# Optimization experiments

Hardware: AMD Instinct MI355X
Metric: run time of the kernel (lower is better)

Reference implementation:

```python
import jax, jax.numpy as jnp
import numpy as np

D_MODEL = 1024
NUM_HEADS = 16


def setup_inputs() -> dict:
    key = jax.random.key(0)
    ks = jax.random.split(key, 5)
    B, S, D = 2, 2048, D_MODEL
    x = jax.random.normal(ks[0], (B, S, D), dtype=jnp.float32)
    # nn.Linear(d_model, d_model, bias=False) weights, shape [out, in]
    scale = 1.0 / np.sqrt(D)
    Wq = jax.random.normal(ks[1], (D, D), dtype=jnp.float32) * scale
    Wk = jax.random.normal(ks[2], (D, D), dtype=jnp.float32) * scale
    Wv = jax.random.normal(ks[3], (D, D), dtype=jnp.float32) * scale
    Wo = jax.random.normal(ks[4], (D, D), dtype=jnp.float32) * scale
    return {"x": x, "Wq": Wq, "Wk": Wk, "Wv": Wv, "Wo": Wo}


def reference(x, Wq, Wk, Wv, Wo):
    B, S, D = x.shape
    H = NUM_HEADS
    dh = D // H
    # projections: x @ W.T (Linear without bias)
    q = (x @ Wq.T).reshape(B, S, H, dh).transpose(0, 2, 1, 3)  # [B,H,S,dh]
    k = (x @ Wk.T).reshape(B, S, H, dh).transpose(0, 2, 1, 3)
    v = (x @ Wv.T).reshape(B, S, H, dh).transpose(0, 2, 1, 3)
    scores = jnp.einsum("bhqd,bhkd->bhqk", q, k) / jnp.sqrt(jnp.float32(dh))
    # causal mask: positions j > i get -inf before softmax
    causal = jnp.triu(jnp.ones((S, S), dtype=bool), k=1)
    scores = jnp.where(causal, -jnp.inf, scores)
    attn = jax.nn.softmax(scores, axis=-1)  # [B,H,S,S]
    out = jnp.einsum("bhqk,bhkd->bhqd", attn, v)  # [B,H,S,dh]
    out = out.transpose(0, 2, 1, 3).reshape(B, S, D)
    return out @ Wo.T
```

## Files before the change

### kernel.cpp

```cpp
#include <hip/hip_runtime.h>

typedef __attribute__((ext_vector_type(8))) __bf16 bf16x8;
typedef __attribute__((ext_vector_type(4))) __bf16 bf16x4;
typedef __attribute__((ext_vector_type(2))) __bf16 bf16x2;
typedef __attribute__((ext_vector_type(4))) float f32x4;
typedef __attribute__((ext_vector_type(16))) float f32x16;
typedef __attribute__((ext_vector_type(4))) unsigned uint4v;

static constexpr int S = 2048;
static constexpr int D = 1024;
static constexpr int BATCH = 2;
static constexpr int M_ROWS = BATCH * S;

#define GLOAD_LDS16(gp, lp)                                                        \
  __builtin_amdgcn_global_load_lds((const __attribute__((address_space(1))) void*)(gp), \
                                   (__attribute__((address_space(3))) void*)(lp), 16, 0, 0)

__global__ __launch_bounds__(256) void cast_f32_bf16(const float* __restrict__ in,
                                                     __bf16* __restrict__ out) {
  int i = (blockIdx.x * 256 + threadIdx.x) * 4;
  *reinterpret_cast<bf16x4*>(out + i) =
      __builtin_convertvector(*reinterpret_cast<const f32x4*>(in + i), bf16x4);
}

__global__ __launch_bounds__(256) void cast_w4(const float* __restrict__ w0, const float* __restrict__ w1,
                                               const float* __restrict__ w2, const float* __restrict__ w3,
                                               __bf16* __restrict__ o0, __bf16* __restrict__ o1,
                                               __bf16* __restrict__ o2, __bf16* __restrict__ o3) {
  const float* in = blockIdx.y == 0 ? w0 : blockIdx.y == 1 ? w1 : blockIdx.y == 2 ? w2 : w3;
  __bf16* out = blockIdx.y == 0 ? o0 : blockIdx.y == 1 ? o1 : blockIdx.y == 2 ? o2 : o3;
  int i = (blockIdx.x * 256 + threadIdx.x) * 4;
  *reinterpret_cast<bf16x4*>(out + i) =
      __builtin_convertvector(*reinterpret_cast<const f32x4*>(in + i), bf16x4);
}

template <typename OutT>
__device__ __forceinline__ void gemm_core(const __bf16* __restrict__ A,
                                          const __bf16* __restrict__ Bm,
                                          OutT* __restrict__ C, int m0, int n0, int K, int ldc,
                                          __bf16* At, __bf16* Bt) {
  const int tid = threadIdx.x;
  const int w = tid >> 6, l = tid & 63;
  const int wr = w >> 1, wc = w & 1;
  const int ln = l & 15, gr = l >> 4;

  const int srow = w * 32 + (l >> 2);
  const int scol = (l & 3) * 8;
  const size_t aoff = (size_t)(m0 + srow) * K + scol;
  const size_t boff = (size_t)(n0 + srow) * K + scol;
  __bf16* lA = At + w * 2 * 512;
  __bf16* lB = Bt + w * 2 * 512;

  f32x4 acc[4][4] = {};

  for (int k0 = 0; k0 < K; k0 += 32) {
    __syncthreads();
    GLOAD_LDS16(A + aoff + k0, lA);
    GLOAD_LDS16(A + aoff + (size_t)16 * K + k0, lA + 512);
    GLOAD_LDS16(Bm + boff + k0, lB);
    GLOAD_LDS16(Bm + boff + (size_t)16 * K + k0, lB + 512);
    __syncthreads();

    bf16x8 af[4], bfr[4];
#pragma unroll
    for (int mi = 0; mi < 4; mi++)
      af[mi] = *reinterpret_cast<const bf16x8*>(&At[(wr * 64 + mi * 16 + ln) * 32 + gr * 8]);
#pragma unroll
    for (int ni = 0; ni < 4; ni++)
      bfr[ni] = *reinterpret_cast<const bf16x8*>(&Bt[(wc * 64 + ni * 16 + ln) * 32 + gr * 8]);
#pragma unroll
    for (int mi = 0; mi < 4; mi++)
#pragma unroll
      for (int ni = 0; ni < 4; ni++)
        acc[mi][ni] = __builtin_amdgcn_mfma_f32_16x16x32_bf16(af[mi], bfr[ni], acc[mi][ni], 0, 0, 0);
  }

#pragma unroll
  for (int mi = 0; mi < 4; mi++)
#pragma unroll
    for (int ni = 0; ni < 4; ni++)
#pragma unroll
      for (int r = 0; r < 4; r++) {
        int row = m0 + wr * 64 + mi * 16 + gr * 4 + r;
        int col = n0 + wc * 64 + ni * 16 + ln;
        float v = acc[mi][ni][r];
        if constexpr (__is_same(OutT, float))
          C[(size_t)row * ldc + col] = v;
        else
          C[(size_t)row * ldc + col] = (__bf16)v;
      }
}

__global__ __launch_bounds__(256) void qkv_gemm(const __bf16* __restrict__ xb,
                                                const __bf16* __restrict__ wq,
                                                const __bf16* __restrict__ wk,
                                                const __bf16* __restrict__ wv,
                                                __bf16* __restrict__ q, __bf16* __restrict__ k,
                                                __bf16* __restrict__ vt) {
  __shared__ __bf16 At[128 * 32];
  __shared__ __bf16 Bt[128 * 32];
  const int id = blockIdx.x;
  const __bf16 *A, *B;
  __bf16* C;
  int m0, n0, ldc;
  if (id < 512) {
    A = xb;
    B = (id < 256) ? wq : wk;
    C = (id < 256) ? q : k;
    int t = id & 255;
    m0 = (t >> 3) * 128;
    n0 = (t & 7) * 128;
    ldc = 1024;
  } else {
    int t = id - 512;
    A = wv;
    B = xb;
    C = vt;
    m0 = (t & 7) * 128;
    n0 = (t >> 3) * 128;
    ldc = 4096;
  }
  gemm_core<__bf16>(A, B, C, m0, n0, 1024, ldc, At, Bt);
}

__global__ __launch_bounds__(256) void wo_gemm(const __bf16* __restrict__ ob,
                                               const __bf16* __restrict__ wo,
                                               float* __restrict__ out) {
  __shared__ __bf16 At[128 * 32];
  __shared__ __bf16 Bt[128 * 32];
  gemm_core<float>(ob, wo, out, blockIdx.y * 128, blockIdx.x * 128, 1024, 1024, At, Bt);
}

__global__ __launch_bounds__(512, 2) void attn_kernel(const __bf16* __restrict__ Qb,
                                                      const __bf16* __restrict__ Kb,
                                                      const __bf16* __restrict__ VTb,
                                                      __bf16* __restrict__ Ob) {
  const int lin = blockIdx.x;
  const int wid = ((lin & 7) << 5) | (lin >> 3);
  const int bh = wid >> 3;
  const int j = wid & 7;
  const int b = bh >> 4, h = bh & 15;

  const int tid = threadIdx.x;
  const int w = tid >> 6, l = tid & 63;
  const int q31 = l & 31, hi = l >> 5;

  int qt;
  switch (w) {
    case 0: qt = j; break;
    case 1: qt = 16 + j; break;
    case 2: qt = 15 - j; break;
    case 3: qt = 31 - j; break;
    case 4: qt = 63 - j; break;
    case 5: qt = 47 - j; break;
    case 6: qt = 48 + j; break;
    default: qt = 32 + j; break;
  }
  const int q0 = qt * 32;
  const int n = qt + 1;

  const __bf16* Qp = Qb + (size_t)b * S * D + h * 64;
  const __bf16* Kp = Kb + (size_t)b * S * D + h * 64;
  const __bf16* Vt = VTb + (size_t)(h * 64) * M_ROWS + b * S;

  const float SCALE2 = 0.125f * 1.44269504f;
  const float NEG = -1e30f;
  const float THR_RAW = 8.0f / SCALE2;

  bf16x8 qf[4];
#pragma unroll
  for (int ds = 0; ds < 4; ds++)
    qf[ds] = *reinterpret_cast<const bf16x8*>(
        Qp + (size_t)(q0 + q31) * D + ds * 16 + hi * 8);

  f32x16 oacc[2] = {};
  float mr = NEG, ls = 0.f;

  auto loadK = [&](bf16x8 (&dst)[4], int kk) {
#pragma unroll
    for (int ds = 0; ds < 4; ds++)
      dst[ds] = *reinterpret_cast<const bf16x8*>(
          Kp + (size_t)(kk + q31) * D + ds * 16 + hi * 8);
  };
  auto loadV = [&](bf16x8 (&dst)[2][2], int kk) {
#pragma unroll
    for (int d0 = 0; d0 < 2; d0++)
#pragma unroll
      for (int ks = 0; ks < 2; ks++)
        dst[d0][ks] = *reinterpret_cast<const bf16x8*>(
            Vt + (size_t)(d0 * 32 + q31) * M_ROWS + kk + ks * 16 + hi * 8);
  };
  auto qk = [&](f32x16& st, bf16x8 (&kf)[4]) {
    f32x16 z = {};
    __builtin_amdgcn_s_setprio(1);
#pragma unroll
    for (int ds = 0; ds < 4; ds++)
      z = __builtin_amdgcn_mfma_f32_32x32x16_bf16(kf[ds], qf[ds], z, 0, 0, 0);
    __builtin_amdgcn_s_setprio(0);
    st = z;
  };

  auto pack2 = [](float x, float y) -> unsigned {
    bf16x2 p;
    p[0] = (__bf16)x;
    p[1] = (__bf16)y;
    return __builtin_bit_cast(unsigned, p);
  };

  auto smpv = [&](f32x16& st, bf16x8 (&vf)[2][2], int t) {
    const bool tail = (t == n - 1);
    float pv[16];
#pragma unroll
    for (int r = 0; r < 16; r++) {
      float v = st[r];
      if (tail) {
        int keyidx = (r & 3) + 8 * (r >> 2) + 4 * hi;
        v = (keyidx <= q31) ? v : NEG;
      }
      pv[r] = v;
    }
    float t8[8], t4[4];
#pragma unroll
    for (int i = 0; i < 8; i++) t8[i] = fmaxf(pv[i], pv[i + 8]);
#pragma unroll
    for (int i = 0; i < 4; i++) t4[i] = fmaxf(t8[i], t8[i + 4]);
    float tm = fmaxf(fmaxf(t4[0], t4[1]), fmaxf(t4[2], t4[3]));
    tm = fmaxf(tm, __shfl_xor(tm, 32));
    if (!__all(tm - mr <= THR_RAW)) {
      float nm = fmaxf(mr, tm);
      float a = __builtin_exp2f((mr - nm) * SCALE2);
      mr = nm;
      ls *= a;
#pragma unroll
      for (int d0 = 0; d0 < 2; d0++)
#pragma unroll
        for (int r = 0; r < 16; r++) oacc[d0][r] *= a;
    }
    const float mrs = mr * SCALE2;
#pragma unroll
    for (int r = 0; r < 16; r++)
      pv[r] = __builtin_exp2f(__builtin_fmaf(pv[r], SCALE2, -mrs));
    float s8[8], s4[4];
#pragma unroll
    for (int i = 0; i < 8; i++) s8[i] = pv[i] + pv[i + 8];
#pragma unroll
    for (int i = 0; i < 4; i++) s4[i] = s8[i] + s8[i + 4];
    float ps = (s4[0] + s4[1]) + (s4[2] + s4[3]);
    ps += __shfl_xor(ps, 32);
    ls += ps;

    unsigned dw[8];
#pragma unroll
    for (int bb = 0; bb < 4; bb++) {
      dw[2 * bb] = pack2(pv[4 * bb], pv[4 * bb + 1]);
      dw[2 * bb + 1] = pack2(pv[4 * bb + 2], pv[4 * bb + 3]);
    }
    __builtin_amdgcn_s_setprio(1);
#pragma unroll
    for (int ks = 0; ks < 2; ks++) {
      unsigned s0 = hi ? dw[4 * ks + 0] : dw[4 * ks + 2];
      unsigned s1 = hi ? dw[4 * ks + 1] : dw[4 * ks + 3];
      unsigned r0 = (unsigned)__shfl_xor((int)s0, 32);
      unsigned r1 = (unsigned)__shfl_xor((int)s1, 32);
      uint4v uv;
      uv.x = hi ? r0 : dw[4 * ks + 0];
      uv.y = hi ? r1 : dw[4 * ks + 1];
      uv.z = hi ? dw[4 * ks + 2] : r0;
      uv.w = hi ? dw[4 * ks + 3] : r1;
      bf16x8 pb = __builtin_bit_cast(bf16x8, uv);
      oacc[0] = __builtin_amdgcn_mfma_f32_32x32x16_bf16(vf[0][ks], pb, oacc[0], 0, 0, 0);
      oacc[1] = __builtin_amdgcn_mfma_f32_32x32x16_bf16(vf[1][ks], pb, oacc[1], 0, 0, 0);
    }
    __builtin_amdgcn_s_setprio(0);
  };

  f32x16 stA, stB;
  bf16x8 kf0[4], kf1[4], vf0[2][2], vf1[2][2];

  loadK(kf0, 0);
  loadV(vf0, 0);
  if (n > 1) {
    loadK(kf1, 32);
    loadV(vf1, 32);
  }
  qk(stA, kf0);

  auto iter_step = [&](f32x16& stCur, f32x16& stNxt, bf16x8 (&kfNxt)[4],
                       bf16x8 (&kfTgt)[4], bf16x8 (&vfCur)[2][2], int t) {
    if (t + 1 < n) qk(stNxt, kfNxt);
    if (t + 2 < n) loadK(kfTgt, 32 * (t + 2));
    smpv(stCur, vfCur, t);
    if (t + 2 < n) loadV(vfCur, 32 * (t + 2));
  };

  int t = 0;
  for (;;) {
    iter_step(stA, stB, kf1, kf0, vf0, t);
    if (++t >= n) break;
    iter_step(stB, stA, kf0, kf1, vf1, t);
    if (++t >= n) break;
  }

  {
    float inv = 1.0f / ls;
    size_t row = (size_t)(b * S + q0 + q31);
#pragma unroll
    for (int d0 = 0; d0 < 2; d0++)
#pragma unroll
      for (int bb = 0; bb < 4; bb++) {
        bf16x4 ov = {(__bf16)(oacc[d0][4 * bb + 0] * inv), (__bf16)(oacc[d0][4 * bb + 1] * inv),
                     (__bf16)(oacc[d0][4 * bb + 2] * inv), (__bf16)(oacc[d0][4 * bb + 3] * inv)};
        *reinterpret_cast<bf16x4*>(Ob + row * D + h * 64 + d0 * 32 + 8 * bb + 4 * hi) = ov;
      }
  }
}

extern "C" void kernel_launch(void* const* d_in, const int* in_sizes, int n_in,
                              void* d_out, int out_size, void* d_ws, size_t ws_size,
                              hipStream_t stream) {
  const float* x = (const float*)d_in[0];
  const float* Wq = (const float*)d_in[1];
  const float* Wk = (const float*)d_in[2];
  const float* Wv = (const float*)d_in[3];
  const float* Wo = (const float*)d_in[4];
  float* out = (float*)d_out;

  char* ws = (char*)d_ws;
  const size_t MB = 1024 * 1024;
  __bf16* xb = (__bf16*)(ws + 0 * MB);
  __bf16* qb = (__bf16*)(ws + 8 * MB);
  __bf16* kb = (__bf16*)(ws + 16 * MB);
  __bf16* vtb = (__bf16*)(ws + 24 * MB);
  __bf16* ob = (__bf16*)(ws + 32 * MB);
  __bf16* wqb = (__bf16*)(ws + 40 * MB);
  __bf16* wkb = (__bf16*)(ws + 42 * MB);
  __bf16* wvb = (__bf16*)(ws + 44 * MB);
  __bf16* wob = (__bf16*)(ws + 46 * MB);

  const int nx = M_ROWS * D;
  const int nw = D * D;

  cast_f32_bf16<<<nx / 4 / 256, 256, 0, stream>>>(x, xb);
  cast_w4<<<dim3(nw / 4 / 256, 4), 256, 0, stream>>>(Wq, Wk, Wv, Wo, wqb, wkb, wvb, wob);

  qkv_gemm<<<768, 256, 0, stream>>>(xb, wqb, wkb, wvb, qb, kb, vtb);

  attn_kernel<<<256, 512, 0, stream>>>(qb, kb, vtb, ob);

  wo_gemm<<<dim3(8, 32), 256, 0, stream>>>(ob, wob, out);
}
```

Baseline: 147.7 us.

## Split each query tile's KV range across two waves and merge via LDS

Each attention query tile's key range is now split between two waves that each run online softmax over half of the key blocks. The halves' partial outputs, max and sum are combined through shared memory after a block barrier. The grid doubles to 512 blocks with 4 query tiles per block, and launch bounds are raised to 4 blocks per CU to add parallelism and shorten the per-wave critical path. In exchange it adds an LDS round trip, a __syncthreads, extra rescaling work, and tighter register pressure from the higher occupancy target.

```diff
diff --git a/kernel.cpp b/kernel.cpp
--- a/kernel.cpp
+++ b/kernel.cpp
@@ -131,33 +131,39 @@
   gemm_core<float>(ob, wo, out, blockIdx.y * 128, blockIdx.x * 128, 1024, 1024, At, Bt);
 }
 
-__global__ __launch_bounds__(512, 2) void attn_kernel(const __bf16* __restrict__ Qb,
+__global__ __launch_bounds__(512, 4) void attn_kernel(const __bf16* __restrict__ Qb,
                                                       const __bf16* __restrict__ Kb,
                                                       const __bf16* __restrict__ VTb,
                                                       __bf16* __restrict__ Ob) {
+  __shared__ float mlds[4][64][34];
+
   const int lin = blockIdx.x;
-  const int wid = ((lin & 7) << 5) | (lin >> 3);
-  const int bh = wid >> 3;
-  const int j = wid & 7;
+  const int xcd = lin & 7;
+  const int idx = lin >> 3;
+  const int bh = xcd * 4 + (idx >> 4);
+  const int i = idx & 15;
   const int b = bh >> 4, h = bh & 15;
 
   const int tid = threadIdx.x;
   const int w = tid >> 6, l = tid & 63;
   const int q31 = l & 31, hi = l >> 5;
 
-  int qt;
+  int qt, half, slot;
   switch (w) {
-    case 0: qt = j; break;
-    case 1: qt = 16 + j; break;
-    case 2: qt = 15 - j; break;
-    case 3: qt = 31 - j; break;
-    case 4: qt = 63 - j; break;
-    case 5: qt = 47 - j; break;
-    case 6: qt = 48 + j; break;
-    default: qt = 32 + j; break;
+    case 0: qt = 2 * i;      half = 0; slot = 0; break;
+    case 1: qt = 2 * i;      half = 1; slot = 0; break;
+    case 2: qt = 2 * i + 1;  half = 0; slot = 1; break;
+    case 3: qt = 2 * i + 1;  half = 1; slot = 1; break;
+    case 4: qt = 63 - 2 * i; half = 1; slot = 2; break;
+    case 5: qt = 63 - 2 * i; half = 0; slot = 2; break;
+    case 6: qt = 62 - 2 * i; half = 1; slot = 3; break;
+    default: qt = 62 - 2 * i; half = 0; slot = 3; break;
   }
   const int q0 = qt * 32;
   const int n = qt + 1;
+  const int n0 = (n + 1) >> 1;
+  const int s0 = half ? n0 : 0;
+  const int cnt = half ? (n - n0) : n0;
 
   const __bf16* Qp = Qb + (size_t)b * S * D + h * 64;
   const __bf16* Kp = Kb + (size_t)b * S * D + h * 64;
@@ -207,8 +213,7 @@
     return __builtin_bit_cast(unsigned, p);
   };
 
-  auto smpv = [&](f32x16& st, bf16x8 (&vf)[2][2], int t) {
-    const bool tail = (t == n - 1);
+  auto smpv = [&](f32x16& st, bf16x8 (&vf)[2][2], bool tail) {
     float pv[16];
 #pragma unroll
     for (int r = 0; r < 16; r++) {
@@ -221,9 +226,9 @@
     }
     float t8[8], t4[4];
 #pragma unroll
-    for (int i = 0; i < 8; i++) t8[i] = fmaxf(pv[i], pv[i + 8]);
-#pragma unroll
-    for (int i = 0; i < 4; i++) t4[i] = fmaxf(t8[i], t8[i + 4]);
+    for (int ii = 0; ii < 8; ii++) t8[ii] = fmaxf(pv[ii], pv[ii + 8]);
+#pragma unroll
+    for (int ii = 0; ii < 4; ii++) t4[ii] = fmaxf(t8[ii], t8[ii + 4]);
     float tm = fmaxf(fmaxf(t4[0], t4[1]), fmaxf(t4[2], t4[3]));
     tm = fmaxf(tm, __shfl_xor(tm, 32));
     if (!__all(tm - mr <= THR_RAW)) {
@@ -242,9 +247,9 @@
       pv[r] = __builtin_exp2f(__builtin_fmaf(pv[r], SCALE2, -mrs));
     float s8[8], s4[4];
 #pragma unroll
-    for (int i = 0; i < 8; i++) s8[i] = pv[i] + pv[i + 8];
-#pragma unroll
-    for (int i = 0; i < 4; i++) s4[i] = s8[i] + s8[i + 4];
+    for (int ii = 0; ii < 8; ii++) s8[ii] = pv[ii] + pv[ii + 8];
+#pragma unroll
+    for (int ii = 0; ii < 4; ii++) s4[ii] = s8[ii] + s8[ii + 4];
     float ps = (s4[0] + s4[1]) + (s4[2] + s4[3]);
     ps += __shfl_xor(ps, 32);
     ls += ps;
@@ -258,10 +263,10 @@
     __builtin_amdgcn_s_setprio(1);
 #pragma unroll
     for (int ks = 0; ks < 2; ks++) {
-      unsigned s0 = hi ? dw[4 * ks + 0] : dw[4 * ks + 2];
-      unsigned s1 = hi ? dw[4 * ks + 1] : dw[4 * ks + 3];
-      unsigned r0 = (unsigned)__shfl_xor((int)s0, 32);
-      unsigned r1 = (unsigned)__shfl_xor((int)s1, 32);
+      unsigned s0v = hi ? dw[4 * ks + 0] : dw[4 * ks + 2];
+      unsigned s1v = hi ? dw[4 * ks + 1] : dw[4 * ks + 3];
+      unsigned r0 = (unsigned)__shfl_xor((int)s0v, 32);
+      unsigned r1 = (unsigned)__shfl_xor((int)s1v, 32);
       uint4v uv;
       uv.x = hi ? r0 : dw[4 * ks + 0];
       uv.y = hi ? r1 : dw[4 * ks + 1];
@@ -277,39 +282,59 @@
   f32x16 stA, stB;
   bf16x8 kf0[4], kf1[4], vf0[2][2], vf1[2][2];
 
-  loadK(kf0, 0);
-  loadV(vf0, 0);
-  if (n > 1) {
-    loadK(kf1, 32);
-    loadV(vf1, 32);
-  }
-  qk(stA, kf0);
-
-  auto iter_step = [&](f32x16& stCur, f32x16& stNxt, bf16x8 (&kfNxt)[4],
-                       bf16x8 (&kfTgt)[4], bf16x8 (&vfCur)[2][2], int t) {
-    if (t + 1 < n) qk(stNxt, kfNxt);
-    if (t + 2 < n) loadK(kfTgt, 32 * (t + 2));
-    smpv(stCur, vfCur, t);
-    if (t + 2 < n) loadV(vfCur, 32 * (t + 2));
-  };
-
-  int t = 0;
-  for (;;) {
-    iter_step(stA, stB, kf1, kf0, vf0, t);
-    if (++t >= n) break;
-    iter_step(stB, stA, kf0, kf1, vf1, t);
-    if (++t >= n) break;
-  }
-
-  {
-    float inv = 1.0f / ls;
+  if (cnt > 0) {
+    loadK(kf0, s0 * 32);
+    loadV(vf0, s0 * 32);
+    if (cnt > 1) {
+      loadK(kf1, (s0 + 1) * 32);
+      loadV(vf1, (s0 + 1) * 32);
+    }
+    qk(stA, kf0);
+
+    auto iter_step = [&](f32x16& stCur, f32x16& stNxt, bf16x8 (&kfNxt)[4],
+                         bf16x8 (&kfTgt)[4], bf16x8 (&vfCur)[2][2], int t) {
+      if (t + 1 < cnt) qk(stNxt, kfNxt);
+      if (t + 2 < cnt) loadK(kfTgt, (s0 + t + 2) * 32);
+      smpv(stCur, vfCur, s0 + t == n - 1);
+      if (t + 2 < cnt) loadV(vfCur, (s0 + t + 2) * 32);
+    };
+
+    int t = 0;
+    for (;;) {
+      iter_step(stA, stB, kf1, kf0, vf0, t);
+      if (++t >= cnt) break;
+      iter_step(stB, stA, kf0, kf1, vf1, t);
+      if (++t >= cnt) break;
+    }
+  }
+
+  if (half == 1) {
+    float* p = &mlds[slot][l][0];
+#pragma unroll
+    for (int r = 0; r < 16; r++) p[r] = oacc[0][r];
+#pragma unroll
+    for (int r = 0; r < 16; r++) p[16 + r] = oacc[1][r];
+    p[32] = mr;
+    p[33] = ls;
+  }
+  __syncthreads();
+  if (half == 0) {
+    const float* p = &mlds[slot][l][0];
+    float mr1 = p[32], ls1 = p[33];
+    float mc = fmaxf(mr, mr1);
+    float a0 = __builtin_exp2f((mr - mc) * SCALE2);
+    float a1 = __builtin_exp2f((mr1 - mc) * SCALE2);
+    float inv = 1.0f / (ls * a0 + ls1 * a1);
+    float f0 = a0 * inv, f1 = a1 * inv;
     size_t row = (size_t)(b * S + q0 + q31);
 #pragma unroll
     for (int d0 = 0; d0 < 2; d0++)
 #pragma unroll
       for (int bb = 0; bb < 4; bb++) {
-        bf16x4 ov = {(__bf16)(oacc[d0][4 * bb + 0] * inv), (__bf16)(oacc[d0][4 * bb + 1] * inv),
-                     (__bf16)(oacc[d0][4 * bb + 2] * inv), (__bf16)(oacc[d0][4 * bb + 3] * inv)};
+        bf16x4 ov;
+#pragma unroll
+        for (int rr = 0; rr < 4; rr++)
+          ov[rr] = (__bf16)(oacc[d0][4 * bb + rr] * f0 + p[d0 * 16 + 4 * bb + rr] * f1);
         *reinterpret_cast<bf16x4*>(Ob + row * D + h * 64 + d0 * 32 + 8 * bb + 4 * hi) = ov;
       }
   }
@@ -345,7 +370,7 @@
 
   qkv_gemm<<<768, 256, 0, stream>>>(xb, wqb, wkb, wvb, qb, kb, vtb);
 
-  attn_kernel<<<256, 512, 0, stream>>>(qb, kb, vtb, ob);
+  attn_kernel<<<512, 512, 0, stream>>>(qb, kb, vtb, ob);
 
   wo_gemm<<<dim3(8, 32), 256, 0, stream>>>(ob, wob, out);
 }
```

Measured after the change: 347.5 us. 2.35x slower.

## Split causal key range into two independent online-softmax streams per wave

Applied to the files above, without the earlier changes.

Each wave now processes the key tiles as two halves with separate running max, sum and output accumulators. Each loop iteration handles one tile from each half, and the two partial results are merged with a log-sum-exp combine at the end. The goal is more instruction-level parallelism, since the two independent MFMA and softmax chains can interleave, replacing the earlier software-pipelined single stream. The cost is more registers for the doubled accumulators and fragments, which could lower occupancy or cause spills. Loads are also now issued just before use rather than a full iteration ahead.

```diff
diff --git a/kernel.cpp b/kernel.cpp
--- a/kernel.cpp
+++ b/kernel.cpp
@@ -158,6 +158,8 @@
   }
   const int q0 = qt * 32;
   const int n = qt + 1;
+  const int na = (n + 1) >> 1;
+  const int nb = n >> 1;
 
   const __bf16* Qp = Qb + (size_t)b * S * D + h * 64;
   const __bf16* Kp = Kb + (size_t)b * S * D + h * 64;
@@ -173,8 +175,8 @@
     qf[ds] = *reinterpret_cast<const bf16x8*>(
         Qp + (size_t)(q0 + q31) * D + ds * 16 + hi * 8);
 
-  f32x16 oacc[2] = {};
-  float mr = NEG, ls = 0.f;
+  f32x16 oaccA[2] = {}, oaccB[2] = {};
+  float mrA = NEG, lsA = 0.f, mrB = NEG, lsB = 0.f;
 
   auto loadK = [&](bf16x8 (&dst)[4], int kk) {
 #pragma unroll
@@ -190,26 +192,20 @@
         dst[d0][ks] = *reinterpret_cast<const bf16x8*>(
             Vt + (size_t)(d0 * 32 + q31) * M_ROWS + kk + ks * 16 + hi * 8);
   };
-  auto qk = [&](f32x16& st, bf16x8 (&kf)[4]) {
+  auto qk1 = [&](f32x16& st, bf16x8 (&kf)[4]) {
     f32x16 z = {};
-    __builtin_amdgcn_s_setprio(1);
 #pragma unroll
     for (int ds = 0; ds < 4; ds++)
       z = __builtin_amdgcn_mfma_f32_32x32x16_bf16(kf[ds], qf[ds], z, 0, 0, 0);
-    __builtin_amdgcn_s_setprio(0);
     st = z;
   };
-
   auto pack2 = [](float x, float y) -> unsigned {
     bf16x2 p;
     p[0] = (__bf16)x;
     p[1] = (__bf16)y;
     return __builtin_bit_cast(unsigned, p);
   };
-
-  auto smpv = [&](f32x16& st, bf16x8 (&vf)[2][2], int t) {
-    const bool tail = (t == n - 1);
-    float pv[16];
+  auto maskmax = [&](f32x16& st, bool tail, float (&pv)[16]) -> float {
 #pragma unroll
     for (int r = 0; r < 16; r++) {
       float v = st[r];
@@ -221,95 +217,121 @@
     }
     float t8[8], t4[4];
 #pragma unroll
-    for (int i = 0; i < 8; i++) t8[i] = fmaxf(pv[i], pv[i + 8]);
-#pragma unroll
-    for (int i = 0; i < 4; i++) t4[i] = fmaxf(t8[i], t8[i + 4]);
+    for (int ii = 0; ii < 8; ii++) t8[ii] = fmaxf(pv[ii], pv[ii + 8]);
+#pragma unroll
+    for (int ii = 0; ii < 4; ii++) t4[ii] = fmaxf(t8[ii], t8[ii + 4]);
     float tm = fmaxf(fmaxf(t4[0], t4[1]), fmaxf(t4[2], t4[3]));
-    tm = fmaxf(tm, __shfl_xor(tm, 32));
-    if (!__all(tm - mr <= THR_RAW)) {
-      float nm = fmaxf(mr, tm);
-      float a = __builtin_exp2f((mr - nm) * SCALE2);
-      mr = nm;
-      ls *= a;
-#pragma unroll
-      for (int d0 = 0; d0 < 2; d0++)
-#pragma unroll
-        for (int r = 0; r < 16; r++) oacc[d0][r] *= a;
-    }
+    return fmaxf(tm, __shfl_xor(tm, 32));
+  };
+  auto rescale = [&](float& mr, float& ls, f32x16& o0, f32x16& o1, float tm) {
+    float nm = fmaxf(mr, tm);
+    float a = __builtin_exp2f((mr - nm) * SCALE2);
+    mr = nm;
+    ls *= a;
+#pragma unroll
+    for (int r = 0; r < 16; r++) o0[r] *= a;
+#pragma unroll
+    for (int r = 0; r < 16; r++) o1[r] *= a;
+  };
+  auto expsum = [&](float (&pv)[16], float mr, float& ls, unsigned (&dw)[8]) {
     const float mrs = mr * SCALE2;
 #pragma unroll
     for (int r = 0; r < 16; r++)
       pv[r] = __builtin_exp2f(__builtin_fmaf(pv[r], SCALE2, -mrs));
     float s8[8], s4[4];
 #pragma unroll
-    for (int i = 0; i < 8; i++) s8[i] = pv[i] + pv[i + 8];
-#pragma unroll
-    for (int i = 0; i < 4; i++) s4[i] = s8[i] + s8[i + 4];
+    for (int ii = 0; ii < 8; ii++) s8[ii] = pv[ii] + pv[ii + 8];
+#pragma unroll
+    for (int ii = 0; ii < 4; ii++) s4[ii] = s8[ii] + s8[ii + 4];
     float ps = (s4[0] + s4[1]) + (s4[2] + s4[3]);
     ps += __shfl_xor(ps, 32);
     ls += ps;
-
-    unsigned dw[8];
 #pragma unroll
     for (int bb = 0; bb < 4; bb++) {
       dw[2 * bb] = pack2(pv[4 * bb], pv[4 * bb + 1]);
       dw[2 * bb + 1] = pack2(pv[4 * bb + 2], pv[4 * bb + 3]);
     }
-    __builtin_amdgcn_s_setprio(1);
+  };
+  auto pvmma = [&](unsigned (&dw)[8], bf16x8 (&vf)[2][2], f32x16& o0, f32x16& o1) {
 #pragma unroll
     for (int ks = 0; ks < 2; ks++) {
-      unsigned s0 = hi ? dw[4 * ks + 0] : dw[4 * ks + 2];
-      unsigned s1 = hi ? dw[4 * ks + 1] : dw[4 * ks + 3];
-      unsigned r0 = (unsigned)__shfl_xor((int)s0, 32);
-      unsigned r1 = (unsigned)__shfl_xor((int)s1, 32);
+      unsigned s0v = hi ? dw[4 * ks + 0] : dw[4 * ks + 2];
+      unsigned s1v = hi ? dw[4 * ks + 1] : dw[4 * ks + 3];
+      unsigned r0 = (unsigned)__shfl_xor((int)s0v, 32);
+      unsigned r1 = (unsigned)__shfl_xor((int)s1v, 32);
       uint4v uv;
       uv.x = hi ? r0 : dw[4 * ks + 0];
       uv.y = hi ? r1 : dw[4 * ks + 1];
       uv.z = hi ? dw[4 * ks + 2] : r0;
       uv.w = hi ? dw[4 * ks + 3] : r1;
       bf16x8 pb = __builtin_bit_cast(bf16x8, uv);
-      oacc[0] = __builtin_amdgcn_mfma_f32_32x32x16_bf16(vf[0][ks], pb, oacc[0], 0, 0, 0);
-      oacc[1] = __builtin_amdgcn_mfma_f32_32x32x16_bf16(vf[1][ks], pb, oacc[1], 0, 0, 0);
+      o0 = __builtin_amdgcn_mfma_f32_32x32x16_bf16(vf[0][ks], pb, o0, 0, 0, 0);
+      o1 = __builtin_amdgcn_mfma_f32_32x32x16_bf16(vf[1][ks], pb, o1, 0, 0, 0);
     }
+  };
+
+  bf16x8 kfA[4], kfB[4], vfA[2][2], vfB[2][2];
+  f32x16 stA, stB;
+
+  loadK(kfA, 0);
+  if (nb > 0) loadK(kfB, na * 32);
+
+  for (int i = 0; i < nb; i++) {
+    loadV(vfA, i * 32);
+    loadV(vfB, (na + i) * 32);
+    __builtin_amdgcn_s_setprio(1);
+    qk1(stA, kfA);
+    qk1(stB, kfB);
     __builtin_amdgcn_s_setprio(0);
-  };
-
-  f32x16 stA, stB;
-  bf16x8 kf0[4], kf1[4], vf0[2][2], vf1[2][2];
-
-  loadK(kf0, 0);
-  loadV(vf0, 0);
-  if (n > 1) {
-    loadK(kf1, 32);
-    loadV(vf1, 32);
-  }
-  qk(stA, kf0);
-
-  auto iter_step = [&](f32x16& stCur, f32x16& stNxt, bf16x8 (&kfNxt)[4],
-                       bf16x8 (&kfTgt)[4], bf16x8 (&vfCur)[2][2], int t) {
-    if (t + 1 < n) qk(stNxt, kfNxt);
-    if (t + 2 < n) loadK(kfTgt, 32 * (t + 2));
-    smpv(stCur, vfCur, t);
-    if (t + 2 < n) loadV(vfCur, 32 * (t + 2));
-  };
-
-  int t = 0;
-  for (;;) {
-    iter_step(stA, stB, kf1, kf0, vf0, t);
-    if (++t >= n) break;
-    iter_step(stB, stA, kf0, kf1, vf1, t);
-    if (++t >= n) break;
+    if (i + 1 < na) loadK(kfA, (i + 1) * 32);
+    if (i + 1 < nb) loadK(kfB, (na + i + 1) * 32);
+
+    float pvA[16], pvB[16];
+    float tmA = maskmax(stA, false, pvA);
+    float tmB = maskmax(stB, i == nb - 1, pvB);
+    if (!__all((tmA - mrA <= THR_RAW) && (tmB - mrB <= THR_RAW))) {
+      rescale(mrA, lsA, oaccA[0], oaccA[1], tmA);
+      rescale(mrB, lsB, oaccB[0], oaccB[1], tmB);
+    }
+    unsigned dwA[8], dwB[8];
+    expsum(pvA, mrA, lsA, dwA);
+    expsum(pvB, mrB, lsB, dwB);
+    __builtin_amdgcn_s_setprio(1);
+    pvmma(dwA, vfA, oaccA[0], oaccA[1]);
+    pvmma(dwB, vfB, oaccB[0], oaccB[1]);
+    __builtin_amdgcn_s_setprio(0);
+  }
+  if (na > nb) {
+    const int i = na - 1;
+    loadV(vfA, i * 32);
+    __builtin_amdgcn_s_setprio(1);
+    qk1(stA, kfA);
+    __builtin_amdgcn_s_setprio(0);
+    float pvA[16];
+    float tmA = maskmax(stA, n == 1, pvA);
+    if (!__all(tmA - mrA <= THR_RAW)) rescale(mrA, lsA, oaccA[0], oaccA[1], tmA);
+    unsigned dwA[8];
+    expsum(pvA, mrA, lsA, dwA);
+    __builtin_amdgcn_s_setprio(1);
+    pvmma(dwA, vfA, oaccA[0], oaccA[1]);
+    __builtin_amdgcn_s_setprio(0);
   }
 
   {
-    float inv = 1.0f / ls;
+    float mc = fmaxf(mrA, mrB);
+    float a0 = __builtin_exp2f((mrA - mc) * SCALE2);
+    float a1 = __builtin_exp2f((mrB - mc) * SCALE2);
+    float inv = 1.0f / (lsA * a0 + lsB * a1);
+    float f0 = a0 * inv, f1 = a1 * inv;
     size_t row = (size_t)(b * S + q0 + q31);
 #pragma unroll
     for (int d0 = 0; d0 < 2; d0++)
 #pragma unroll
       for (int bb = 0; bb < 4; bb++) {
-        bf16x4 ov = {(__bf16)(oacc[d0][4 * bb + 0] * inv), (__bf16)(oacc[d0][4 * bb + 1] * inv),
-                     (__bf16)(oacc[d0][4 * bb + 2] * inv), (__bf16)(oacc[d0][4 * bb + 3] * inv)};
+        bf16x4 ov;
+#pragma unroll
+        for (int rr = 0; rr < 4; rr++)
+          ov[rr] = (__bf16)(oaccA[d0][4 * bb + rr] * f0 + oaccB[d0][4 * bb + rr] * f1);
         *reinterpret_cast<bf16x4*>(Ob + row * D + h * 64 + d0 * 32 + 8 * bb + 4 * hi) = ov;
       }
   }
```

Measured after the change: 142.4 us. 1.04x faster.
